# Kernel tuning notes

Measured on AMD Instinct MI355X. Metric: run time of the kernel, lower is better.

The kernel has to match this reference:

```python
import jax, jax.numpy as jnp
import numpy as np

E = 2048   # embed_dim
H = 16     # num query heads
D = E // H # head_dim = 128
B = 2
S = 2048


def setup_inputs() -> dict:
    key = jax.random.key(0)
    ks = jax.random.split(key, 12)
    sc = 0.02
    return {
        "input": jax.random.normal(ks[0], (B, S, E), jnp.float32),
        "kv": jax.random.normal(ks[1], (B, S, E), jnp.float32),
        "Wq": jax.random.normal(ks[2], (E, E), jnp.float32) * sc,
        "bq": jnp.zeros((E,), jnp.float32),
        "Wk": jax.random.normal(ks[3], (D, E), jnp.float32) * sc,
        "bk": jnp.zeros((D,), jnp.float32),
        "Wv": jax.random.normal(ks[4], (D, E), jnp.float32) * sc,
        "bv": jnp.zeros((D,), jnp.float32),
        "Wo": jax.random.normal(ks[5], (E, E), jnp.float32) * sc,
        "bo": jnp.zeros((E,), jnp.float32),
        "expanding_context": 0,
    }


def reference(input, kv, Wq, bq, Wk, bk, Wv, bv, Wo, bo, expanding_context):
    b, s, _ = input.shape
    # projections (torch Linear: x @ W.T + b)
    q = (input @ Wq.T + bq).reshape(b, s, H, D).transpose(0, 2, 1, 3)  # [B,H,S,D]
    k = kv @ Wk.T + bk  # [B,S,D] single KV head
    v = kv @ Wv.T + bv  # [B,S,D]
    # scores with single KV head broadcast across query heads
    scores = jnp.einsum('bhsd,btd->bhst', q, k) / jnp.sqrt(jnp.float32(D))
    causal = jnp.triu(jnp.ones((s, s), bool), k=1)  # True above diagonal
    scores = jnp.where(causal[None, None], jnp.float32(-jnp.inf), scores)
    attn = jax.nn.softmax(scores, axis=-1)
    out = jnp.einsum('bhst,btd->bhsd', attn, v)  # [B,H,S,D]
    out = out.transpose(0, 2, 1, 3).reshape(b, s, E)
    return out @ Wo.T + bo
```

## Files before the change

kernel.cpp:

```cpp
#include <hip/hip_runtime.h>

#define B_  2
#define S_  2048
#define E_  2048
#define H_  16
#define D_  128
#define BS_ (B_*S_)

typedef __bf16 bf16_t;
typedef __bf16 bf16x8 __attribute__((ext_vector_type(8)));
typedef __bf16 bf16x4 __attribute__((ext_vector_type(4)));
typedef float  f32x4  __attribute__((ext_vector_type(4)));

#define QSCALE 0.1275174131003543f

__device__ __forceinline__ void gld16(const bf16_t* g, bf16_t* l) {
    __builtin_amdgcn_global_load_lds(
        (const __attribute__((address_space(1))) void*)g,
        (__attribute__((address_space(3))) void*)l,
        16, 0, 0);
}

__global__ void cvt_all(const float* __restrict__ s0, const float* __restrict__ s1,
                        const float* __restrict__ s2, const float* __restrict__ s3,
                        const float* __restrict__ s4, const float* __restrict__ s5,
                        bf16_t* d0, bf16_t* d1, bf16_t* d2,
                        bf16_t* d3, bf16_t* d4, bf16_t* d5)
{
    long i = ((long)blockIdx.x * blockDim.x + threadIdx.x) * 4;
    const float* s; bf16_t* d;
    if      (i <  8388608) { s = s0; d = d0; }
    else if (i < 16777216) { s = s1; d = d1; i -=  8388608; }
    else if (i < 20971520) { s = s2; d = d2; i -= 16777216; }
    else if (i < 21233664) { s = s3; d = d3; i -= 20971520; }
    else if (i < 21495808) { s = s4; d = d4; i -= 21233664; }
    else                   { s = s5; d = d5; i -= 21495808; }
    float4 v = *(const float4*)(s + i);
    bf16x4 o;
    o[0] = (bf16_t)v.x; o[1] = (bf16_t)v.y; o[2] = (bf16_t)v.z; o[3] = (bf16_t)v.w;
    *(bf16x4*)(d + i) = o;
}

__global__ __launch_bounds__(256) void gemm_bt(
    const bf16_t* __restrict__ A, const bf16_t* __restrict__ W,
    const float* __restrict__ biasA, const float* __restrict__ biasB,
    float* __restrict__ Cf, bf16_t* __restrict__ Cb,
    int M, int N, int K, float scale)
{
    __shared__ __align__(16) bf16_t As[128 * 64];
    __shared__ __align__(16) bf16_t Bs[128 * 64];

    const int tid  = threadIdx.x;
    const int wave = tid >> 6, lane = tid & 63;
    const int wm = wave >> 1, wn = wave & 1;
    const int lrow = lane & 15, quad = lane >> 4;
    const int m0 = blockIdx.y * 128, n0 = blockIdx.x * 128;
    const int r8 = lane >> 3, c8 = (lane & 7) << 3;

    f32x4 acc[4][4] = {};

    for (int k0 = 0; k0 < K; k0 += 64) {
        __syncthreads();
#pragma unroll
        for (int j = 0; j < 4; ++j) {
            int base = (wave * 4 + j) * 8;
            gld16(A + (size_t)(m0 + base + r8) * K + k0 + c8, &As[base * 64]);
            gld16(W + (size_t)(n0 + base + r8) * K + k0 + c8, &Bs[base * 64]);
        }
        __syncthreads();
#pragma unroll
        for (int ks = 0; ks < 2; ++ks) {
            bf16x8 af[4], bfr[4];
#pragma unroll
            for (int mt = 0; mt < 4; ++mt)
                af[mt] = *(const bf16x8*)&As[(wm * 64 + mt * 16 + lrow) * 64 + ks * 32 + quad * 8];
#pragma unroll
            for (int nt = 0; nt < 4; ++nt)
                bfr[nt] = *(const bf16x8*)&Bs[(wn * 64 + nt * 16 + lrow) * 64 + ks * 32 + quad * 8];
#pragma unroll
            for (int mt = 0; mt < 4; ++mt)
#pragma unroll
                for (int nt = 0; nt < 4; ++nt)
                    acc[mt][nt] = __builtin_amdgcn_mfma_f32_16x16x32_bf16(
                        af[mt], bfr[nt], acc[mt][nt], 0, 0, 0);
        }
    }

#pragma unroll
    for (int mt = 0; mt < 4; ++mt) {
#pragma unroll
        for (int nt = 0; nt < 4; ++nt) {
            int col = n0 + wn * 64 + nt * 16 + lrow;
            const float* bp = biasA; int ci = col;
            if (biasB && col >= 128) { bp = biasB; ci = col - 128; }
            float bv = bp[ci];
#pragma unroll
            for (int r = 0; r < 4; ++r) {
                int row = m0 + wm * 64 + mt * 16 + quad * 4 + r;
                float v = (acc[mt][nt][r] + bv) * scale;
                if (Cf) Cf[(size_t)row * N + col] = v;
                else    Cb[(size_t)row * N + col] = (bf16_t)v;
            }
        }
    }
}

__global__ __launch_bounds__(512, 4) void mqa_attn(
    const bf16_t* __restrict__ Q, const bf16_t* __restrict__ KV,
    bf16_t* __restrict__ O)
{
    __shared__ __align__(16) bf16_t Kt[64][136];
    __shared__ __align__(16) bf16_t Vt[128][72];
    __shared__ __align__(16) bf16_t Pl[8][16][72];

    const int qb = 15 - blockIdx.x;
    const int h = blockIdx.y, b = blockIdx.z;
    const int tid = threadIdx.x, wave = tid >> 6, lane = tid & 63;
    const int lrow = lane & 15, quad = lane >> 4;
    const int q0 = qb * 128 + wave * 16;

    bf16x8 qf[4];
    {
        const bf16_t* qp = Q + ((size_t)(b * S_ + q0 + lrow)) * E_ + h * D_ + quad * 8;
#pragma unroll
        for (int ks = 0; ks < 4; ++ks) qf[ks] = *(const bf16x8*)(qp + ks * 32);
    }

    f32x4 oacc[8] = {};
    float rs[4] = {0.f, 0.f, 0.f, 0.f};

    const int ntiles = 2 * qb + 2;
    for (int kt = 0; kt < ntiles; ++kt) {
        const int k_base = kt * 64;
        __syncthreads();
#pragma unroll
        for (int i = 0; i < 2; ++i) {
            int c = tid + 512 * i;
            int row = c >> 4, cc = (c & 15) << 3;
            *(uint4*)&Kt[row][cc] =
                *(const uint4*)(KV + ((size_t)(b * S_ + k_base + row)) * 256 + cc);
        }
#pragma unroll
        for (int i = 0; i < 2; ++i) {
            int c = tid + 512 * i;
            int n = c & 63, d0 = (c >> 6) << 3;
            bf16x8 v = *(const bf16x8*)(KV + ((size_t)(b * S_ + k_base + n)) * 256 + 128 + d0);
#pragma unroll
            for (int j = 0; j < 8; ++j) Vt[d0 + j][n] = v[j];
        }
        __syncthreads();

        if (k_base <= q0 + 15) {
            f32x4 sc[4] = {};
#pragma unroll
            for (int ks = 0; ks < 4; ++ks) {
                bf16x8 a = qf[ks];
#pragma unroll
                for (int c = 0; c < 4; ++c) {
                    bf16x8 kb = *(const bf16x8*)&Kt[c * 16 + lrow][ks * 32 + quad * 8];
                    sc[c] = __builtin_amdgcn_mfma_f32_16x16x32_bf16(a, kb, sc[c], 0, 0, 0);
                }
            }
            const bool diag = (k_base + 63 > q0);
#pragma unroll
            for (int c = 0; c < 4; ++c) {
#pragma unroll
                for (int r = 0; r < 4; ++r) {
                    float s = sc[c][r];
                    if (diag) {
                        int kj = k_base + c * 16 + lrow;
                        int qi = q0 + quad * 4 + r;
                        if (kj > qi) s = -1e30f;
                    }
                    float p = exp2f(fminf(s, 110.f));
                    rs[r] += p;
                    Pl[wave][quad * 4 + r][c * 16 + lrow] = (bf16_t)p;
                }
            }
#pragma unroll
            for (int ks = 0; ks < 2; ++ks) {
                bf16x8 ap = *(const bf16x8*)&Pl[wave][lrow][ks * 32 + quad * 8];
#pragma unroll
                for (int dt = 0; dt < 8; ++dt) {
                    bf16x8 bv = *(const bf16x8*)&Vt[dt * 16 + lrow][ks * 32 + quad * 8];
                    oacc[dt] = __builtin_amdgcn_mfma_f32_16x16x32_bf16(ap, bv, oacc[dt], 0, 0, 0);
                }
            }
        }
    }

#pragma unroll
    for (int off = 8; off >= 1; off >>= 1)
#pragma unroll
        for (int r = 0; r < 4; ++r) rs[r] += __shfl_xor(rs[r], off, 16);
#pragma unroll
    for (int r = 0; r < 4; ++r) {
        float inv = 1.0f / rs[r];
        int row = q0 + quad * 4 + r;
#pragma unroll
        for (int dt = 0; dt < 8; ++dt)
            O[((size_t)(b * S_ + row)) * E_ + h * D_ + dt * 16 + lrow] =
                (bf16_t)(oacc[dt][r] * inv);
    }
}

extern "C" void kernel_launch(void* const* d_in, const int* in_sizes, int n_in,
                              void* d_out, int out_size, void* d_ws, size_t ws_size,
                              hipStream_t stream)
{
    const float* x   = (const float*)d_in[0];
    const float* kv  = (const float*)d_in[1];
    const float* Wq  = (const float*)d_in[2];
    const float* bq  = (const float*)d_in[3];
    const float* Wk  = (const float*)d_in[4];
    const float* bk  = (const float*)d_in[5];
    const float* Wv  = (const float*)d_in[6];
    const float* bv  = (const float*)d_in[7];
    const float* Wo  = (const float*)d_in[8];
    const float* bo  = (const float*)d_in[9];
    float* out = (float*)d_out;

    bf16_t* p    = (bf16_t*)d_ws;
    bf16_t* xb   = p;  p += (size_t)BS_ * E_;
    bf16_t* kvb  = p;  p += (size_t)BS_ * E_;
    bf16_t* Wqb  = p;  p += (size_t)E_ * E_;
    bf16_t* Wkvb = p;  p += (size_t)2 * D_ * E_;
    bf16_t* Wob  = p;  p += (size_t)E_ * E_;
    bf16_t* Qb   = p;  p += (size_t)BS_ * E_;
    bf16_t* KVb  = p;  p += (size_t)BS_ * 256;
    bf16_t* Ob   = p;  p += (size_t)BS_ * E_;

    cvt_all<<<dim3(25088), dim3(256), 0, stream>>>(
        x, kv, Wq, Wk, Wv, Wo,
        xb, kvb, Wqb, Wkvb, Wkvb + (size_t)D_ * E_, Wob);

    gemm_bt<<<dim3(E_ / 128, BS_ / 128), 256, 0, stream>>>(
        xb, Wqb, bq, nullptr, nullptr, Qb, BS_, E_, E_, QSCALE);
    gemm_bt<<<dim3(2, BS_ / 128), 256, 0, stream>>>(
        kvb, Wkvb, bk, bv, nullptr, KVb, BS_, 256, E_, 1.0f);

    mqa_attn<<<dim3(S_ / 128, H_, B_), 512, 0, stream>>>(Qb, KVb, Ob);

    gemm_bt<<<dim3(E_ / 128, BS_ / 128), 256, 0, stream>>>(
        Ob, Wob, bo, nullptr, out, nullptr, BS_, E_, E_, 1.0f);
}
```

Before: 426.2 us.

## Merge Q and KV projection GEMMs, prefetch KV tiles, balance attention block order

New measurement: 365.7 us. 14.2% less time.

```diff
diff --git a/kernel.cpp b/kernel.cpp
--- a/kernel.cpp
+++ b/kernel.cpp
@@ -41,20 +41,17 @@
     *(bf16x4*)(d + i) = o;
 }
 
-__global__ __launch_bounds__(256) void gemm_bt(
+__device__ __forceinline__ void gemm_tile(
     const bf16_t* __restrict__ A, const bf16_t* __restrict__ W,
     const float* __restrict__ biasA, const float* __restrict__ biasB,
     float* __restrict__ Cf, bf16_t* __restrict__ Cb,
-    int M, int N, int K, float scale)
-{
-    __shared__ __align__(16) bf16_t As[128 * 64];
-    __shared__ __align__(16) bf16_t Bs[128 * 64];
-
+    int N, int K, float scale, int m0, int n0,
+    bf16_t* As, bf16_t* Bs)
+{
     const int tid  = threadIdx.x;
     const int wave = tid >> 6, lane = tid & 63;
     const int wm = wave >> 1, wn = wave & 1;
     const int lrow = lane & 15, quad = lane >> 4;
-    const int m0 = blockIdx.y * 128, n0 = blockIdx.x * 128;
     const int r8 = lane >> 3, c8 = (lane & 7) << 3;
 
     f32x4 acc[4][4] = {};
@@ -105,6 +102,35 @@
     }
 }
 
+__global__ __launch_bounds__(256) void gemm_qkv(
+    const bf16_t* __restrict__ xb, const bf16_t* __restrict__ kvb,
+    const bf16_t* __restrict__ Wq, const bf16_t* __restrict__ Wkv,
+    const float* __restrict__ bq, const float* __restrict__ bk,
+    const float* __restrict__ bv,
+    bf16_t* __restrict__ Qb, bf16_t* __restrict__ KVb)
+{
+    __shared__ __align__(16) bf16_t As[128 * 64];
+    __shared__ __align__(16) bf16_t Bs[128 * 64];
+    const int m0 = blockIdx.y * 128;
+    if (blockIdx.x < 16) {
+        gemm_tile(xb, Wq, bq, nullptr, nullptr, Qb, E_, E_, QSCALE,
+                  m0, blockIdx.x * 128, As, Bs);
+    } else {
+        gemm_tile(kvb, Wkv, bk, bv, nullptr, KVb, 256, E_, 1.0f,
+                  m0, (blockIdx.x - 16) * 128, As, Bs);
+    }
+}
+
+__global__ __launch_bounds__(256) void gemm_o(
+    const bf16_t* __restrict__ A, const bf16_t* __restrict__ W,
+    const float* __restrict__ bias, float* __restrict__ Cf)
+{
+    __shared__ __align__(16) bf16_t As[128 * 64];
+    __shared__ __align__(16) bf16_t Bs[128 * 64];
+    gemm_tile(A, W, bias, nullptr, Cf, nullptr, E_, E_, 1.0f,
+              blockIdx.y * 128, blockIdx.x * 128, As, Bs);
+}
+
 __global__ __launch_bounds__(512, 4) void mqa_attn(
     const bf16_t* __restrict__ Q, const bf16_t* __restrict__ KV,
     bf16_t* __restrict__ O)
@@ -113,12 +139,14 @@
     __shared__ __align__(16) bf16_t Vt[128][72];
     __shared__ __align__(16) bf16_t Pl[8][16][72];
 
-    const int qb = 15 - blockIdx.x;
-    const int h = blockIdx.y, b = blockIdx.z;
+    const int bx = blockIdx.x, h = blockIdx.y, b = blockIdx.z;
+    const int qb = b ? bx : (15 - bx);
     const int tid = threadIdx.x, wave = tid >> 6, lane = tid & 63;
     const int lrow = lane & 15, quad = lane >> 4;
     const int q0 = qb * 128 + wave * 16;
 
+    const bf16_t* kvp = KV + (size_t)(b * S_) * 256;
+
     bf16x8 qf[4];
     {
         const bf16_t* qp = Q + ((size_t)(b * S_ + q0 + lrow)) * E_ + h * D_ + quad * 8;
@@ -130,25 +158,36 @@
     float rs[4] = {0.f, 0.f, 0.f, 0.f};
 
     const int ntiles = 2 * qb + 2;
+    bf16x8 kreg[2], vreg[2];
+
+#pragma unroll
+    for (int i = 0; i < 2; ++i) {
+        int c = tid + 512 * i;
+        kreg[i] = *(const bf16x8*)(kvp + (size_t)(c >> 4) * 256 + ((c & 15) << 3));
+        vreg[i] = *(const bf16x8*)(kvp + (size_t)(c & 63) * 256 + 128 + ((c >> 6) << 3));
+    }
+
     for (int kt = 0; kt < ntiles; ++kt) {
         const int k_base = kt * 64;
         __syncthreads();
 #pragma unroll
         for (int i = 0; i < 2; ++i) {
             int c = tid + 512 * i;
-            int row = c >> 4, cc = (c & 15) << 3;
-            *(uint4*)&Kt[row][cc] =
-                *(const uint4*)(KV + ((size_t)(b * S_ + k_base + row)) * 256 + cc);
-        }
-#pragma unroll
-        for (int i = 0; i < 2; ++i) {
-            int c = tid + 512 * i;
+            *(bf16x8*)&Kt[c >> 4][(c & 15) << 3] = kreg[i];
             int n = c & 63, d0 = (c >> 6) << 3;
-            bf16x8 v = *(const bf16x8*)(KV + ((size_t)(b * S_ + k_base + n)) * 256 + 128 + d0);
-#pragma unroll
-            for (int j = 0; j < 8; ++j) Vt[d0 + j][n] = v[j];
-        }
-        __syncthreads();
+#pragma unroll
+            for (int j = 0; j < 8; ++j) Vt[d0 + j][n] = vreg[i][j];
+        }
+        __syncthreads();
+        if (kt + 1 < ntiles) {
+            const int nb = (kt + 1) * 64;
+#pragma unroll
+            for (int i = 0; i < 2; ++i) {
+                int c = tid + 512 * i;
+                kreg[i] = *(const bf16x8*)(kvp + (size_t)(nb + (c >> 4)) * 256 + ((c & 15) << 3));
+                vreg[i] = *(const bf16x8*)(kvp + (size_t)(nb + (c & 63)) * 256 + 128 + ((c >> 6) << 3));
+            }
+        }
 
         if (k_base <= q0 + 15) {
             f32x4 sc[4] = {};
@@ -234,13 +273,10 @@
         x, kv, Wq, Wk, Wv, Wo,
         xb, kvb, Wqb, Wkvb, Wkvb + (size_t)D_ * E_, Wob);
 
-    gemm_bt<<<dim3(E_ / 128, BS_ / 128), 256, 0, stream>>>(
-        xb, Wqb, bq, nullptr, nullptr, Qb, BS_, E_, E_, QSCALE);
-    gemm_bt<<<dim3(2, BS_ / 128), 256, 0, stream>>>(
-        kvb, Wkvb, bk, bv, nullptr, KVb, BS_, 256, E_, 1.0f);
+    gemm_qkv<<<dim3(18, BS_ / 128), 256, 0, stream>>>(
+        xb, kvb, Wqb, Wkvb, bq, bk, bv, Qb, KVb);
 
     mqa_attn<<<dim3(S_ / 128, H_, B_), 512, 0, stream>>>(Qb, KVb, Ob);
 
-    gemm_bt<<<dim3(E_ / 128, BS_ / 128), 256, 0, stream>>>(
-        Ob, Wob, bo, nullptr, out, nullptr, BS_, E_, E_, 1.0f);
-}
+    gemm_o<<<dim3(E_ / 128, BS_ / 128), 256, 0, stream>>>(Ob, Wob, bo, out);
+}
```
